# Performance work log

Hardware: AMD Instinct MI355X
Metric: run time of the kernel (lower is better)

## Reference

```python
import jax, jax.numpy as jnp
import numpy as np

B, L, H = 16, 2048, 1024
N = B * L
K_SEL = 8192
LN_EPS = 1e-12
PD_EPS = 1e-6  # torch f.pairwise_distance default eps


def setup_inputs() -> dict:
    key = jax.random.key(0)
    k1, k2, k3, k4 = jax.random.split(key, 4)
    msp = jax.random.normal(k1, (B, L, H), dtype=jnp.float32)
    lab = jax.random.normal(k2, (B, L, H), dtype=jnp.float32)
    # mask with exactly K_SEL true positions (static compaction size)
    perm = jax.random.permutation(k3, N)[:K_SEL]
    mask = jnp.zeros((N,), dtype=bool).at[perm].set(True).reshape(B, L)
    dense_w = jax.random.normal(k4, (H, H), dtype=jnp.float32) / np.sqrt(H)
    return {
        "masked_sentence_prediction": msp,
        "label_embeddings": lab,
        "label_mask": mask,
        "dense_w": dense_w,
        "dense_b": jnp.zeros((H,), dtype=jnp.float32),
        "ln_gamma": jnp.ones((H,), dtype=jnp.float32),
        "ln_beta": jnp.zeros((H,), dtype=jnp.float32),
        "K": K_SEL,
    }


def reference(masked_sentence_prediction, label_embeddings, label_mask,
              dense_w, dense_b, ln_gamma, ln_beta, K):
    Hd = masked_sentence_prediction.shape[-1]
    mask_flat = label_mask.reshape(-1)
    # stream compaction: rows where mask is true (static size K)
    idx = jnp.nonzero(mask_flat, size=K)[0]
    preds = masked_sentence_prediction.reshape(-1, Hd)[idx]      # [K, H]
    labels = label_embeddings.reshape(-1, Hd)[idx]               # [K, H]
    # dense + LayerNorm
    h = preds @ dense_w.T + dense_b
    mu = jnp.mean(h, axis=-1, keepdims=True)
    var = jnp.mean(jnp.square(h - mu), axis=-1, keepdims=True)
    h = (h - mu) * jax.lax.rsqrt(var + LN_EPS) * ln_gamma + ln_beta
    # contrastive logits against dynamic sentence vocabulary
    logits = h @ labels.T                                        # [K, K]
    log_probs = jax.nn.log_softmax(logits, axis=1)
    probs = jnp.exp(log_probs)
    eye = jnp.eye(K, dtype=logits.dtype)
    per_example_loss_distance = jnp.sum(jnp.abs(probs - eye + PD_EPS), axis=1)
    per_example_loss_product = -jnp.diagonal(log_probs)
    denom = K + 1e-5
    loss_distance = jnp.sum(per_example_loss_distance) / denom
    loss_product = jnp.sum(per_example_loss_product) / denom
    loss_variance_distance = jnp.var(per_example_loss_distance, ddof=1)
    loss_variance_product = jnp.var(per_example_loss_product, ddof=1)
    return (logits, per_example_loss_distance, per_example_loss_product,
            loss_distance, loss_product, loss_variance_distance, loss_variance_product)
```

## Files before the change

### kernel.cpp

```cpp
#include <hip/hip_runtime.h>
#include <cstdint>

#define NROWS 32768
#define HD    1024
#define KSEL  8192
#define LN_EPS 1e-12f
#define PD_EPS 1e-6f

typedef unsigned short u16;
typedef __bf16 bf16x8 __attribute__((ext_vector_type(8)));
typedef float  f32x4  __attribute__((ext_vector_type(4)));

__device__ inline u16 f2bf(float f) {
    union { float f; uint32_t u; } x; x.f = f;
    uint32_t r = (x.u + 0x7fffu + ((x.u >> 16) & 1u)) >> 16;
    return (u16)r;
}

__device__ inline uint2 pack4(float a, float b, float c, float d) {
    uint2 r;
    r.x = (uint32_t)f2bf(a) | ((uint32_t)f2bf(b) << 16);
    r.y = (uint32_t)f2bf(c) | ((uint32_t)f2bf(d) << 16);
    return r;
}

__global__ void compact_mask_k(const uint8_t* mb, const int32_t* mi, int* idx) {
    __shared__ int cnt[1024];
    __shared__ int tmp[1024];
    __shared__ int mode_s;
    const int t = threadIdx.x;
    const int per = NROWS / 1024;
    const int base = t * per;
    int c0 = 0;
    for (int i = 0; i < per; ++i) c0 += (mb[base + i] != 0);
    tmp[t] = c0;
    __syncthreads();
    for (int off = 512; off > 0; off >>= 1) {
        if (t < off) tmp[t] += tmp[t + off];
        __syncthreads();
    }
    if (t == 0) mode_s = (tmp[0] == KSEL) ? 0 : 1;
    __syncthreads();
    const int mode = mode_s;
    int c = c0;
    if (mode) { c = 0; for (int i = 0; i < per; ++i) c += (mi[base + i] != 0); }
    cnt[t] = c;
    __syncthreads();
    for (int off = 1; off < 1024; off <<= 1) {
        int add = (t >= off) ? cnt[t - off] : 0;
        __syncthreads();
        cnt[t] += add;
        __syncthreads();
    }
    int pos = cnt[t] - c;
    for (int i = 0; i < per; ++i) {
        bool v = mode ? (mi[base + i] != 0) : (mb[base + i] != 0);
        if (v) idx[pos++] = base + i;
    }
}

__global__ void gather_conv_k(const float* __restrict__ msp, const float* __restrict__ lab,
                              const int* __restrict__ idx, const float* __restrict__ W,
                              u16* __restrict__ predsB, u16* __restrict__ labelsB,
                              u16* __restrict__ Wb) {
    const int b = blockIdx.x;
    const int t = threadIdx.x;
    if (b < KSEL) {
        const int src = idx[b];
        float4 p = *(const float4*)(msp + (size_t)src * HD + t * 4);
        float4 q = *(const float4*)(lab + (size_t)src * HD + t * 4);
        *(uint2*)(predsB  + (size_t)b * HD + t * 4) = pack4(p.x, p.y, p.z, p.w);
        *(uint2*)(labelsB + (size_t)b * HD + t * 4) = pack4(q.x, q.y, q.z, q.w);
    } else {
        const int i = ((b - KSEL) * 256 + t) * 4;
        float4 v = *(const float4*)(W + i);
        *(uint2*)(Wb + i) = pack4(v.x, v.y, v.z, v.w);
    }
}

#define STAGE(XPTR, ROWBASE, KT, I, LBASE) do {                                      \
    const int f_ = (I) * 512 + tid;                                                  \
    const int r_ = f_ >> 3;                                                          \
    const int sp_ = (f_ & 7) ^ (r_ & 7);                                             \
    const u16* g_ = (XPTR) + (size_t)((ROWBASE) + r_) * Kd + koff + (KT) * 64 + sp_ * 8; \
    __builtin_amdgcn_global_load_lds(                                                \
        (const __attribute__((address_space(1))) void*)g_,                           \
        (__attribute__((address_space(3))) void*)(lds + (LBASE) + f_ * 8), 16, 0, 0);\
} while (0)

#define GEMM_PRO_AND_KLOOP(TVAL)                                                      \
    const int nx  = N >> 8;                                                           \
    int wg  = ((nwg & 7) == 0) ? ((bid & 7) * (nwg >> 3) + (bid >> 3)) : bid;         \
    const int bm = wg / nx, bn = wg % nx;                                             \
    const size_t brow = (size_t)bm << 8, bcol = (size_t)bn << 8;                      \
    const int tid = threadIdx.x;                                                      \
    const int l = tid & 63, wid = tid >> 6;                                           \
    const int wm = wid >> 2, wn = wid & 3;                                            \
    const int lr = l & 15, lq = l >> 4;                                               \
    const int sw = lr & 7;                                                            \
    f32x4 acc[8][4] = {};                                                             \
    const int arow = (wm * 128 + lr) * 64;                                            \
    const int brow2 = (wn * 64 + lr) * 64;                                            \
    const int s0 = (lq ^ sw) * 8;                                                     \
    const int s1 = ((4 + lq) ^ sw) * 8;                                               \
    _Pragma("unroll")                                                                 \
    for (int i = 0; i < 4; ++i) STAGE(A,  brow, 0, i, 0);                             \
    _Pragma("unroll")                                                                 \
    for (int i = 0; i < 4; ++i) STAGE(Bt, bcol, 0, i, 49152);                         \
    _Pragma("unroll")                                                                 \
    for (int i = 0; i < 4; ++i) STAGE(A,  brow, 1, i, 16384);                         \
    asm volatile("s_waitcnt vmcnt(4)" ::: "memory");                                  \
    __builtin_amdgcn_s_barrier();                                                     \
    const int T = (TVAL);                                                             \
    int abi = 0;                                                                      \
    _Pragma("unroll 1")                                                               \
    for (int t = 0; t < T; ++t) {                                                     \
        const int aB = abi * 16384;                                                   \
        const int bB = 49152 + (t & 1) * 16384;                                       \
        const int aN = (abi >= 1 ? abi - 1 : 2) * 16384;                              \
        const int bN = 49152 + ((t + 1) & 1) * 16384;                                 \
        bf16x8 a0[8], b0[4], a1[8], b1[4];                                            \
                     \
        _Pragma("unroll")                                                             \
        for (int mi = 0; mi < 8; ++mi)                                                \
            a0[mi] = *(const bf16x8*)(lds + aB + arow + mi * 1024 + s0);              \
        _Pragma("unroll")                                                             \
        for (int ni = 0; ni < 4; ++ni)                                                \
            b0[ni] = *(const bf16x8*)(lds + bB + brow2 + ni * 1024 + s0);             \
        _Pragma("unroll")                                                             \
        for (int mi = 0; mi < 8; ++mi)                                                \
            a1[mi] = *(const bf16x8*)(lds + aB + arow + mi * 1024 + s1);              \
        _Pragma("unroll")                                                             \
        for (int ni = 0; ni < 4; ++ni)                                                \
            b1[ni] = *(const bf16x8*)(lds + bB + brow2 + ni * 1024 + s1);             \
                      \
        if (t + 1 < T) {                                                              \
            STAGE(Bt, bcol, t + 1, 0, bN); STAGE(Bt, bcol, t + 1, 1, bN);             \
            STAGE(Bt, bcol, t + 1, 2, bN); STAGE(Bt, bcol, t + 1, 3, bN);             \
        }                                                                             \
        if (t + 2 < T) {                                                              \
            STAGE(A, brow, t + 2, 0, aN); STAGE(A, brow, t + 2, 1, aN);               \
            STAGE(A, brow, t + 2, 2, aN); STAGE(A, brow, t + 2, 3, aN);               \
        }                                                                             \
                     \
        _Pragma("unroll")                                                             \
        for (int mi = 0; mi < 8; ++mi) {                                              \
            _Pragma("unroll")                                                         \
            for (int ni = 0; ni < 4; ++ni)                                            \
                acc[mi][ni] = __builtin_amdgcn_mfma_f32_16x16x32_bf16(a0[mi], b0[ni], acc[mi][ni], 0, 0, 0); \
        }                                                                             \
        _Pragma("unroll")                                                             \
        for (int mi = 0; mi < 8; ++mi) {                                              \
            _Pragma("unroll")                                                         \
            for (int ni = 0; ni < 4; ++ni)                                            \
                acc[mi][ni] = __builtin_amdgcn_mfma_f32_16x16x32_bf16(a1[mi], b1[ni], acc[mi][ni], 0, 0, 0); \
        }                                                                             \
                      \
        if (t < T - 2) { asm volatile("s_waitcnt vmcnt(4)" ::: "memory"); }           \
        else           { asm volatile("s_waitcnt vmcnt(0)" ::: "memory"); }           \
        __builtin_amdgcn_s_barrier();                                                 \
        abi = (abi == 2) ? 0 : abi + 1;                                               \
    }

__global__ __launch_bounds__(512, 2)
void gemm256a_k(const u16* __restrict__ A, const u16* __restrict__ Bt,
                float* __restrict__ C, int M, int N, int Kd) {
    extern __shared__ u16 lds[];
    const int nwg = (M >> 8) * (N >> 8);
    int bid = blockIdx.x;
    const int half = (bid >= nwg) ? 1 : 0;
    if (half) bid -= nwg;
    const int KdH = Kd >> 1;
    const int koff = half * KdH;
    float* Cp = C + (size_t)half * ((size_t)M * N);
    GEMM_PRO_AND_KLOOP(KdH >> 6);
    #pragma unroll
    for (int m = 0; m < 8; ++m) {
        const size_t rb = brow + wm * 128 + m * 16 + lq * 4;
        #pragma unroll
        for (int n = 0; n < 4; ++n) {
            const size_t cb = bcol + wn * 64 + n * 16 + lr;
            #pragma unroll
            for (int rr = 0; rr < 4; ++rr)
                Cp[(rb + rr) * (size_t)N + cb] = acc[m][n][rr];
        }
    }
}

__global__ __launch_bounds__(512, 2)
void gemm256s_k(const u16* __restrict__ A, const u16* __restrict__ Bt,
                float* __restrict__ C, int M, int N, int Kd,
                float2* __restrict__ pst) {
    extern __shared__ u16 lds[];
    const int nwg = (M >> 8) * (N >> 8);
    int bid = blockIdx.x;
    const int koff = 0;
    GEMM_PRO_AND_KLOOP(Kd >> 6);

    float2* sbuf = (float2*)lds;
    #pragma unroll
    for (int m = 0; m < 8; ++m) {
        #pragma unroll
        for (int rr = 0; rr < 4; ++rr) {
            float v0 = acc[m][0][rr], v1 = acc[m][1][rr];
            float v2 = acc[m][2][rr], v3 = acc[m][3][rr];
            float mx = fmaxf(fmaxf(v0, v1), fmaxf(v2, v3));
            #pragma unroll
            for (int o = 1; o < 16; o <<= 1) mx = fmaxf(mx, __shfl_xor(mx, o));
            float se = __expf(v0 - mx) + __expf(v1 - mx) + __expf(v2 - mx) + __expf(v3 - mx);
            #pragma unroll
            for (int o = 1; o < 16; o <<= 1) se += __shfl_xor(se, o);
            if (lr == 0) {
                const int rl = wm * 128 + m * 16 + lq * 4 + rr;
                sbuf[rl * 5 + wn] = make_float2(mx, se);
            }
        }
        const size_t rb = brow + wm * 128 + m * 16 + lq * 4;
        #pragma unroll
        for (int n = 0; n < 4; ++n) {
            const size_t cb = bcol + wn * 64 + n * 16 + lr;
            #pragma unroll
            for (int rr = 0; rr < 4; ++rr)
                C[(rb + rr) * (size_t)N + cb] = acc[m][n][rr];
        }
    }
    asm volatile("s_waitcnt lgkmcnt(0)" ::: "memory");
    __builtin_amdgcn_s_barrier();
    if (tid < 256) {
        const float2 p0 = sbuf[tid * 5 + 0], p1 = sbuf[tid * 5 + 1];
        const float2 p2 = sbuf[tid * 5 + 2], p3 = sbuf[tid * 5 + 3];
        const float M2 = fmaxf(fmaxf(p0.x, p1.x), fmaxf(p2.x, p3.x));
        const float S2 = p0.y * __expf(p0.x - M2) + p1.y * __expf(p1.x - M2)
                       + p2.y * __expf(p2.x - M2) + p3.y * __expf(p3.x - M2);
        pst[(brow + tid) * (N >> 8) + bn] = make_float2(M2, S2);
    }
}

__global__ __launch_bounds__(256)
void loss_final_k(const float2* __restrict__ pst, const float* __restrict__ logits,
                  float* __restrict__ peld, float* __restrict__ pelp) {
    const int tid = threadIdx.x;
    const int wv = tid >> 6, half = (tid & 63) >> 5, l5 = tid & 31;
    const int row = blockIdx.x * 8 + wv * 2 + half;
    const float2 p = pst[(size_t)row * 32 + l5];
    const float d = logits[(size_t)row * (KSEL + 1)];
    float M = p.x;
    #pragma unroll
    for (int o = 1; o < 32; o <<= 1) M = fmaxf(M, __shfl_xor(M, o));
    float S = p.y * __expf(p.x - M);
    #pragma unroll
    for (int o = 1; o < 32; o <<= 1) S += __shfl_xor(S, o);
    if (l5 == 0) {
        const float pi = __expf(d - M) / S;
        peld[row] = 2.0f - 2.0f * pi + (float)(KSEL - 2) * PD_EPS;
        pelp[row] = M + __logf(S) - d;
    }
}

__device__ inline float blockSum(float v, float* red) {
    #pragma unroll
    for (int o = 32; o > 0; o >>= 1) v += __shfl_down(v, o);
    __syncthreads();
    if ((threadIdx.x & 63) == 0) red[threadIdx.x >> 6] = v;
    __syncthreads();
    return red[0] + red[1] + red[2] + red[3];
}

__global__ void ln_k(const float* __restrict__ Hp0, const float* __restrict__ Hp1,
                     const float* __restrict__ bias,
                     const float* __restrict__ gamma, const float* __restrict__ beta,
                     u16* __restrict__ Hb) {
    __shared__ float red[4];
    const int r = blockIdx.x, t = threadIdx.x;
    float4 x4 = *(const float4*)(Hp0 + (size_t)r * HD + t * 4);
    float4 y4 = *(const float4*)(Hp1 + (size_t)r * HD + t * 4);
    float4 b4 = *(const float4*)(bias + t * 4);
    float x[4] = { x4.x + y4.x + b4.x, x4.y + y4.y + b4.y,
                   x4.z + y4.z + b4.z, x4.w + y4.w + b4.w };
    float s = x[0] + x[1] + x[2] + x[3];
    float mu = blockSum(s, red) * (1.0f / HD);
    float d0 = x[0] - mu, d1 = x[1] - mu, d2 = x[2] - mu, d3 = x[3] - mu;
    float vs = d0 * d0 + d1 * d1 + d2 * d2 + d3 * d3;
    float var = blockSum(vs, red) * (1.0f / HD);
    float rs = rsqrtf(var + LN_EPS);
    float4 g4 = *(const float4*)(gamma + t * 4);
    float4 e4 = *(const float4*)(beta + t * 4);
    float y0 = d0 * rs * g4.x + e4.x;
    float y1 = d1 * rs * g4.y + e4.y;
    float y2 = d2 * rs * g4.z + e4.z;
    float y3 = d3 * rs * g4.w + e4.w;
    *(uint2*)(Hb + (size_t)r * HD + t * 4) = pack4(y0, y1, y2, y3);
}

__global__ __launch_bounds__(1024)
void reduce_k(const float* __restrict__ peld, const float* __restrict__ pelp,
              float* __restrict__ scalars) {
    __shared__ double red[4][16];
    const int t = threadIdx.x;
    double a = 0.0, b = 0.0, c = 0.0, d = 0.0;
    for (int i = t; i < KSEL; i += 1024) {
        const double pd = (double)peld[i];
        const double pp = (double)pelp[i];
        a += pd; b += pd * pd; c += pp; d += pp * pp;
    }
    #pragma unroll
    for (int o = 32; o > 0; o >>= 1) {
        a += __shfl_down(a, o); b += __shfl_down(b, o);
        c += __shfl_down(c, o); d += __shfl_down(d, o);
    }
    const int wv = t >> 6;
    if ((t & 63) == 0) { red[0][wv] = a; red[1][wv] = b; red[2][wv] = c; red[3][wv] = d; }
    __syncthreads();
    if (t == 0) {
        double s1 = 0, s2 = 0, s3 = 0, s4 = 0;
        #pragma unroll
        for (int i = 0; i < 16; ++i) { s1 += red[0][i]; s2 += red[1][i]; s3 += red[2][i]; s4 += red[3][i]; }
        const double Kd = (double)KSEL;
        const double denom = Kd + 1e-5;
        scalars[0] = (float)(s1 / denom);
        scalars[1] = (float)(s3 / denom);
        scalars[2] = (float)((s2 - s1 * s1 / Kd) / (Kd - 1.0));
        scalars[3] = (float)((s4 - s3 * s3 / Kd) / (Kd - 1.0));
    }
}

extern "C" void kernel_launch(void* const* d_in, const int* in_sizes, int n_in,
                              void* d_out, int out_size, void* d_ws, size_t ws_size,
                              hipStream_t stream) {
    const float* msp   = (const float*)d_in[0];
    const float* lab   = (const float*)d_in[1];
    const void*  mask  = d_in[2];
    const float* W     = (const float*)d_in[3];
    const float* bias  = (const float*)d_in[4];
    const float* gamma = (const float*)d_in[5];
    const float* beta  = (const float*)d_in[6];
    float* out = (float*)d_out;
    char*  ws  = (char*)d_ws;

    int*    idx     = (int*)ws;
    float2* pst     = (float2*)(ws + 65536);
    u16*    wBf     = (u16*)(ws + 65536);
    u16*    labelsB = (u16*)(ws + (size_t)(4  << 20));
    u16*    hB      = (u16*)(ws + (size_t)(20 << 20));
    u16*    predsB  = (u16*)d_out;
    float*  hPre    = out + ((size_t)8 << 20);

    float* peld    = out + (size_t)KSEL * KSEL;
    float* pelp    = peld + KSEL;
    float* scalars = pelp + KSEL;

    hipFuncSetAttribute(reinterpret_cast<const void*>(&gemm256a_k),
                        hipFuncAttributeMaxDynamicSharedMemorySize, 163840);
    hipFuncSetAttribute(reinterpret_cast<const void*>(&gemm256s_k),
                        hipFuncAttributeMaxDynamicSharedMemorySize, 163840);

    compact_mask_k<<<1, 1024, 0, stream>>>((const uint8_t*)mask, (const int32_t*)mask, idx);
    gather_conv_k<<<KSEL + 1024, 256, 0, stream>>>(msp, lab, idx, W, predsB, labelsB, wBf);
    gemm256a_k<<<2 * (KSEL / 256) * (HD / 256), 512, 163840, stream>>>(
        predsB, wBf, hPre, KSEL, HD, HD);
    ln_k<<<KSEL, 256, 0, stream>>>(hPre, hPre + (size_t)KSEL * HD, bias, gamma, beta, hB);
    gemm256s_k<<<(KSEL / 256) * (KSEL / 256), 512, 163840, stream>>>(
        hB, labelsB, out, KSEL, KSEL, HD, pst);
    loss_final_k<<<KSEL / 8, 256, 0, stream>>>(pst, out, peld, pelp);
    reduce_k<<<1, 1024, 0, stream>>>(peld, pelp, scalars);
}
```

Before: 266.7 us.

## Run logits GEMM in FP8 e4m3 instead of bf16

Normalized hidden states and label embeddings are now packed to FP8 e4m3 rather than bf16, and the KxK logits GEMM uses fp8 MFMA with K-tiles of 128 bytes per row. The shared GEMM macro is inlined into the dense GEMM and a separate FP8 staging and loop path is written for the logits GEMM. The aim is to halve the bytes moved and raise MFMA throughput for the dominant GEMM. In exchange, logits precision drops sharply, which risks the accuracy of the outputs and the softmax-derived losses.

```diff
diff --git a/kernel.cpp b/kernel.cpp
--- a/kernel.cpp
+++ b/kernel.cpp
@@ -22,6 +22,34 @@
     r.x = (uint32_t)f2bf(a) | ((uint32_t)f2bf(b) << 16);
     r.y = (uint32_t)f2bf(c) | ((uint32_t)f2bf(d) << 16);
     return r;
+}
+
+__device__ inline uint32_t enc_e4m3(float f) {
+    union { float f; uint32_t u; } x; x.f = f;
+    uint32_t s = (x.u >> 31) << 7;
+    float a = fabsf(f);
+    if (a >= 448.f) return s | 0x7e;
+    if (a < 0.001953125f) {
+        int q = (int)(a * 512.f + 0.5f);
+        return s | (uint32_t)q;
+    }
+    int e; float m = frexpf(a, &e);
+    int E = e - 1 + 7;
+    int q = (int)((m * 2.f - 1.f) * 8.f + 0.5f);
+    if (q == 8) { q = 0; E += 1; }
+    if (E >= 16) return s | 0x7e;
+    if (E <= 0) { int qq = (int)(a * 512.f + 0.5f); return s | (uint32_t)qq; }
+    return s | (uint32_t)(E << 3) | (uint32_t)q;
+}
+
+__device__ inline uint32_t pack4_f8(float a, float b, float c, float d) {
+#if defined(__has_builtin) && __has_builtin(__builtin_amdgcn_cvt_pk_fp8_f32)
+    int v = __builtin_amdgcn_cvt_pk_fp8_f32(a, b, 0, false);
+    v = __builtin_amdgcn_cvt_pk_fp8_f32(c, d, v, true);
+    return (uint32_t)v;
+#else
+    return enc_e4m3(a) | (enc_e4m3(b) << 8) | (enc_e4m3(c) << 16) | (enc_e4m3(d) << 24);
+#endif
 }
 
 __global__ void compact_mask_k(const uint8_t* mb, const int32_t* mi, int* idx) {
@@ -61,7 +89,7 @@
 
 __global__ void gather_conv_k(const float* __restrict__ msp, const float* __restrict__ lab,
                               const int* __restrict__ idx, const float* __restrict__ W,
-                              u16* __restrict__ predsB, u16* __restrict__ labelsB,
+                              u16* __restrict__ predsB, uint8_t* __restrict__ labelsB8,
                               u16* __restrict__ Wb) {
     const int b = blockIdx.x;
     const int t = threadIdx.x;
@@ -69,8 +97,8 @@
         const int src = idx[b];
         float4 p = *(const float4*)(msp + (size_t)src * HD + t * 4);
         float4 q = *(const float4*)(lab + (size_t)src * HD + t * 4);
-        *(uint2*)(predsB  + (size_t)b * HD + t * 4) = pack4(p.x, p.y, p.z, p.w);
-        *(uint2*)(labelsB + (size_t)b * HD + t * 4) = pack4(q.x, q.y, q.z, q.w);
+        *(uint2*)(predsB + (size_t)b * HD + t * 4) = pack4(p.x, p.y, p.z, p.w);
+        *(uint32_t*)(labelsB8 + (size_t)b * HD + t * 4) = pack4_f8(q.x, q.y, q.z, q.w);
     } else {
         const int i = ((b - KSEL) * 256 + t) * 4;
         float4 v = *(const float4*)(W + i);
@@ -87,80 +115,6 @@
         (const __attribute__((address_space(1))) void*)g_,                           \
         (__attribute__((address_space(3))) void*)(lds + (LBASE) + f_ * 8), 16, 0, 0);\
 } while (0)
-
-#define GEMM_PRO_AND_KLOOP(TVAL)                                                      \
-    const int nx  = N >> 8;                                                           \
-    int wg  = ((nwg & 7) == 0) ? ((bid & 7) * (nwg >> 3) + (bid >> 3)) : bid;         \
-    const int bm = wg / nx, bn = wg % nx;                                             \
-    const size_t brow = (size_t)bm << 8, bcol = (size_t)bn << 8;                      \
-    const int tid = threadIdx.x;                                                      \
-    const int l = tid & 63, wid = tid >> 6;                                           \
-    const int wm = wid >> 2, wn = wid & 3;                                            \
-    const int lr = l & 15, lq = l >> 4;                                               \
-    const int sw = lr & 7;                                                            \
-    f32x4 acc[8][4] = {};                                                             \
-    const int arow = (wm * 128 + lr) * 64;                                            \
-    const int brow2 = (wn * 64 + lr) * 64;                                            \
-    const int s0 = (lq ^ sw) * 8;                                                     \
-    const int s1 = ((4 + lq) ^ sw) * 8;                                               \
-    _Pragma("unroll")                                                                 \
-    for (int i = 0; i < 4; ++i) STAGE(A,  brow, 0, i, 0);                             \
-    _Pragma("unroll")                                                                 \
-    for (int i = 0; i < 4; ++i) STAGE(Bt, bcol, 0, i, 49152);                         \
-    _Pragma("unroll")                                                                 \
-    for (int i = 0; i < 4; ++i) STAGE(A,  brow, 1, i, 16384);                         \
-    asm volatile("s_waitcnt vmcnt(4)" ::: "memory");                                  \
-    __builtin_amdgcn_s_barrier();                                                     \
-    const int T = (TVAL);                                                             \
-    int abi = 0;                                                                      \
-    _Pragma("unroll 1")                                                               \
-    for (int t = 0; t < T; ++t) {                                                     \
-        const int aB = abi * 16384;                                                   \
-        const int bB = 49152 + (t & 1) * 16384;                                       \
-        const int aN = (abi >= 1 ? abi - 1 : 2) * 16384;                              \
-        const int bN = 49152 + ((t + 1) & 1) * 16384;                                 \
-        bf16x8 a0[8], b0[4], a1[8], b1[4];                                            \
-                     \
-        _Pragma("unroll")                                                             \
-        for (int mi = 0; mi < 8; ++mi)                                                \
-            a0[mi] = *(const bf16x8*)(lds + aB + arow + mi * 1024 + s0);              \
-        _Pragma("unroll")                                                             \
-        for (int ni = 0; ni < 4; ++ni)                                                \
-            b0[ni] = *(const bf16x8*)(lds + bB + brow2 + ni * 1024 + s0);             \
-        _Pragma("unroll")                                                             \
-        for (int mi = 0; mi < 8; ++mi)                                                \
-            a1[mi] = *(const bf16x8*)(lds + aB + arow + mi * 1024 + s1);              \
-        _Pragma("unroll")                                                             \
-        for (int ni = 0; ni < 4; ++ni)                                                \
-            b1[ni] = *(const bf16x8*)(lds + bB + brow2 + ni * 1024 + s1);             \
-                      \
-        if (t + 1 < T) {                                                              \
-            STAGE(Bt, bcol, t + 1, 0, bN); STAGE(Bt, bcol, t + 1, 1, bN);             \
-            STAGE(Bt, bcol, t + 1, 2, bN); STAGE(Bt, bcol, t + 1, 3, bN);             \
-        }                                                                             \
-        if (t + 2 < T) {                                                              \
-            STAGE(A, brow, t + 2, 0, aN); STAGE(A, brow, t + 2, 1, aN);               \
-            STAGE(A, brow, t + 2, 2, aN); STAGE(A, brow, t + 2, 3, aN);               \
-        }                                                                             \
-                     \
-        _Pragma("unroll")                                                             \
-        for (int mi = 0; mi < 8; ++mi) {                                              \
-            _Pragma("unroll")                                                         \
-            for (int ni = 0; ni < 4; ++ni)                                            \
-                acc[mi][ni] = __builtin_amdgcn_mfma_f32_16x16x32_bf16(a0[mi], b0[ni], acc[mi][ni], 0, 0, 0); \
-        }                                                                             \
-        _Pragma("unroll")                                                             \
-        for (int mi = 0; mi < 8; ++mi) {                                              \
-            _Pragma("unroll")                                                         \
-            for (int ni = 0; ni < 4; ++ni)                                            \
-                acc[mi][ni] = __builtin_amdgcn_mfma_f32_16x16x32_bf16(a1[mi], b1[ni], acc[mi][ni], 0, 0, 0); \
-        }                                                                             \
-                      \
-        if (t < T - 2) { asm volatile("s_waitcnt vmcnt(4)" ::: "memory"); }           \
-        else           { asm volatile("s_waitcnt vmcnt(0)" ::: "memory"); }           \
-        __builtin_amdgcn_s_barrier();                                                 \
-        abi = (abi == 2) ? 0 : abi + 1;                                               \
-    }
 
 __global__ __launch_bounds__(512, 2)
 void gemm256a_k(const u16* __restrict__ A, const u16* __restrict__ Bt,
@@ -173,7 +127,75 @@
     const int KdH = Kd >> 1;
     const int koff = half * KdH;
     float* Cp = C + (size_t)half * ((size_t)M * N);
-    GEMM_PRO_AND_KLOOP(KdH >> 6);
+
+    const int nx  = N >> 8;
+    int wg  = ((nwg & 7) == 0) ? ((bid & 7) * (nwg >> 3) + (bid >> 3)) : bid;
+    const int bm = wg / nx, bn = wg % nx;
+    const size_t brow = (size_t)bm << 8, bcol = (size_t)bn << 8;
+    const int tid = threadIdx.x;
+    const int l = tid & 63, wid = tid >> 6;
+    const int wm = wid >> 2, wn = wid & 3;
+    const int lr = l & 15, lq = l >> 4;
+    const int sw = lr & 7;
+    f32x4 acc[8][4] = {};
+    const int arow = (wm * 128 + lr) * 64;
+    const int brow2 = (wn * 64 + lr) * 64;
+    const int s0 = (lq ^ sw) * 8;
+    const int s1 = ((4 + lq) ^ sw) * 8;
+    #pragma unroll
+    for (int i = 0; i < 4; ++i) STAGE(A,  brow, 0, i, 0);
+    #pragma unroll
+    for (int i = 0; i < 4; ++i) STAGE(Bt, bcol, 0, i, 49152);
+    #pragma unroll
+    for (int i = 0; i < 4; ++i) STAGE(A,  brow, 1, i, 16384);
+    asm volatile("s_waitcnt vmcnt(4)" ::: "memory");
+    __builtin_amdgcn_s_barrier();
+    const int T = KdH >> 6;
+    int abi = 0;
+    #pragma unroll 1
+    for (int t = 0; t < T; ++t) {
+        const int aB = abi * 16384;
+        const int bB = 49152 + (t & 1) * 16384;
+        const int aN = (abi >= 1 ? abi - 1 : 2) * 16384;
+        const int bN = 49152 + ((t + 1) & 1) * 16384;
+        bf16x8 a0[8], b0[4], a1[8], b1[4];
+        #pragma unroll
+        for (int mi = 0; mi < 8; ++mi)
+            a0[mi] = *(const bf16x8*)(lds + aB + arow + mi * 1024 + s0);
+        #pragma unroll
+        for (int ni = 0; ni < 4; ++ni)
+            b0[ni] = *(const bf16x8*)(lds + bB + brow2 + ni * 1024 + s0);
+        #pragma unroll
+        for (int mi = 0; mi < 8; ++mi)
+            a1[mi] = *(const bf16x8*)(lds + aB + arow + mi * 1024 + s1);
+        #pragma unroll
+        for (int ni = 0; ni < 4; ++ni)
+            b1[ni] = *(const bf16x8*)(lds + bB + brow2 + ni * 1024 + s1);
+        if (t + 1 < T) {
+            STAGE(Bt, bcol, t + 1, 0, bN); STAGE(Bt, bcol, t + 1, 1, bN);
+            STAGE(Bt, bcol, t + 1, 2, bN); STAGE(Bt, bcol, t + 1, 3, bN);
+        }
+        if (t + 2 < T) {
+            STAGE(A, brow, t + 2, 0, aN); STAGE(A, brow, t + 2, 1, aN);
+            STAGE(A, brow, t + 2, 2, aN); STAGE(A, brow, t + 2, 3, aN);
+        }
+        #pragma unroll
+        for (int mi = 0; mi < 8; ++mi) {
+            #pragma unroll
+            for (int ni = 0; ni < 4; ++ni)
+                acc[mi][ni] = __builtin_amdgcn_mfma_f32_16x16x32_bf16(a0[mi], b0[ni], acc[mi][ni], 0, 0, 0);
+        }
+        #pragma unroll
+        for (int mi = 0; mi < 8; ++mi) {
+            #pragma unroll
+            for (int ni = 0; ni < 4; ++ni)
+                acc[mi][ni] = __builtin_amdgcn_mfma_f32_16x16x32_bf16(a1[mi], b1[ni], acc[mi][ni], 0, 0, 0);
+        }
+        if (t < T - 2) { asm volatile("s_waitcnt vmcnt(4)" ::: "memory"); }
+        else           { asm volatile("s_waitcnt vmcnt(0)" ::: "memory"); }
+        __builtin_amdgcn_s_barrier();
+        abi = (abi == 2) ? 0 : abi + 1;
+    }
     #pragma unroll
     for (int m = 0; m < 8; ++m) {
         const size_t rb = brow + wm * 128 + m * 16 + lq * 4;
@@ -187,17 +209,90 @@
     }
 }
 
+#define STAGE8(XPTR, ROWBASE, KT, I, LBASE) do {                                     \
+    const int f_ = (I) * 512 + tid;                                                  \
+    const int r_ = f_ >> 3;                                                          \
+    const int sp_ = (f_ & 7) ^ (r_ & 7);                                             \
+    const uint8_t* g_ = (XPTR) + (size_t)((ROWBASE) + r_) * Kd + (KT) * 128 + sp_ * 16; \
+    __builtin_amdgcn_global_load_lds(                                                \
+        (const __attribute__((address_space(1))) void*)g_,                           \
+        (__attribute__((address_space(3))) void*)(lds8 + (LBASE) + f_ * 16), 16, 0, 0);\
+} while (0)
+
 __global__ __launch_bounds__(512, 2)
-void gemm256s_k(const u16* __restrict__ A, const u16* __restrict__ Bt,
+void gemm256s_k(const uint8_t* __restrict__ A, const uint8_t* __restrict__ Bt,
                 float* __restrict__ C, int M, int N, int Kd,
                 float2* __restrict__ pst) {
     extern __shared__ u16 lds[];
-    const int nwg = (M >> 8) * (N >> 8);
+    uint8_t* lds8 = (uint8_t*)lds;
+    const int nx  = N >> 8;
+    const int nwg = (M >> 8) * nx;
     int bid = blockIdx.x;
-    const int koff = 0;
-    GEMM_PRO_AND_KLOOP(Kd >> 6);
-
-    float2* sbuf = (float2*)lds;
+    int wg  = ((nwg & 7) == 0) ? ((bid & 7) * (nwg >> 3) + (bid >> 3)) : bid;
+    const int bm = wg / nx, bn = wg % nx;
+    const size_t brow = (size_t)bm << 8, bcol = (size_t)bn << 8;
+    const int tid = threadIdx.x;
+    const int l = tid & 63, wid = tid >> 6;
+    const int wm = wid >> 2, wn = wid & 3;
+    const int lr = l & 15, lq = l >> 4;
+    const int sw = lr & 7;
+    f32x4 acc[8][4] = {};
+    const int arow = (wm * 128 + lr) * 128;
+    const int brow2 = (wn * 64 + lr) * 128;
+    int fo[4];
+    #pragma unroll
+    for (int kk = 0; kk < 4; ++kk)
+        fo[kk] = (((kk * 2 + (lq >> 1)) ^ sw) * 16) + (lq & 1) * 8;
+
+    #pragma unroll
+    for (int i = 0; i < 4; ++i) STAGE8(A,  brow, 0, i, 0);
+    #pragma unroll
+    for (int i = 0; i < 4; ++i) STAGE8(Bt, bcol, 0, i, 98304);
+    #pragma unroll
+    for (int i = 0; i < 4; ++i) STAGE8(A,  brow, 1, i, 32768);
+    asm volatile("s_waitcnt vmcnt(4)" ::: "memory");
+    __builtin_amdgcn_s_barrier();
+
+    const int T = Kd >> 7;
+    int abi = 0;
+    #pragma unroll 1
+    for (int t = 0; t < T; ++t) {
+        const int aB = abi * 32768;
+        const int bB = 98304 + (t & 1) * 32768;
+        const int aN = (abi >= 1 ? abi - 1 : 2) * 32768;
+        const int bN = 98304 + ((t + 1) & 1) * 32768;
+        if (t + 1 < T) {
+            STAGE8(Bt, bcol, t + 1, 0, bN); STAGE8(Bt, bcol, t + 1, 1, bN);
+            STAGE8(Bt, bcol, t + 1, 2, bN); STAGE8(Bt, bcol, t + 1, 3, bN);
+        }
+        if (t + 2 < T) {
+            STAGE8(A, brow, t + 2, 0, aN); STAGE8(A, brow, t + 2, 1, aN);
+            STAGE8(A, brow, t + 2, 2, aN); STAGE8(A, brow, t + 2, 3, aN);
+        }
+        #pragma unroll
+        for (int kk = 0; kk < 4; ++kk) {
+            long a[8], b[4];
+            #pragma unroll
+            for (int mi = 0; mi < 8; ++mi)
+                a[mi] = *(const long*)(lds8 + aB + arow + mi * 2048 + fo[kk]);
+            #pragma unroll
+            for (int ni = 0; ni < 4; ++ni)
+                b[ni] = *(const long*)(lds8 + bB + brow2 + ni * 2048 + fo[kk]);
+            #pragma unroll
+            for (int mi = 0; mi < 8; ++mi) {
+                #pragma unroll
+                for (int ni = 0; ni < 4; ++ni)
+                    acc[mi][ni] = __builtin_amdgcn_mfma_f32_16x16x32_fp8_fp8(
+                        a[mi], b[ni], acc[mi][ni], 0, 0, 0);
+            }
+        }
+        if (t < T - 2) { asm volatile("s_waitcnt vmcnt(4)" ::: "memory"); }
+        else           { asm volatile("s_waitcnt vmcnt(0)" ::: "memory"); }
+        __builtin_amdgcn_s_barrier();
+        abi = (abi == 2) ? 0 : abi + 1;
+    }
+
+    float2* sbuf = (float2*)lds8;
     #pragma unroll
     for (int m = 0; m < 8; ++m) {
         #pragma unroll
@@ -269,7 +364,7 @@
 __global__ void ln_k(const float* __restrict__ Hp0, const float* __restrict__ Hp1,
                      const float* __restrict__ bias,
                      const float* __restrict__ gamma, const float* __restrict__ beta,
-                     u16* __restrict__ Hb) {
+                     uint8_t* __restrict__ Hb8) {
     __shared__ float red[4];
     const int r = blockIdx.x, t = threadIdx.x;
     float4 x4 = *(const float4*)(Hp0 + (size_t)r * HD + t * 4);
@@ -289,7 +384,7 @@
     float y1 = d1 * rs * g4.y + e4.y;
     float y2 = d2 * rs * g4.z + e4.z;
     float y3 = d3 * rs * g4.w + e4.w;
-    *(uint2*)(Hb + (size_t)r * HD + t * 4) = pack4(y0, y1, y2, y3);
+    *(uint32_t*)(Hb8 + (size_t)r * HD + t * 4) = pack4_f8(y0, y1, y2, y3);
 }
 
 __global__ __launch_bounds__(1024)
@@ -337,13 +432,13 @@
     float* out = (float*)d_out;
     char*  ws  = (char*)d_ws;
 
-    int*    idx     = (int*)ws;
-    float2* pst     = (float2*)(ws + 65536);
-    u16*    wBf     = (u16*)(ws + 65536);
-    u16*    labelsB = (u16*)(ws + (size_t)(4  << 20));
-    u16*    hB      = (u16*)(ws + (size_t)(20 << 20));
-    u16*    predsB  = (u16*)d_out;
-    float*  hPre    = out + ((size_t)8 << 20);
+    int*     idx      = (int*)ws;
+    float2*  pst      = (float2*)(ws + 65536);
+    u16*     wBf      = (u16*)(ws + 65536);
+    uint8_t* labelsB8 = (uint8_t*)(ws + (size_t)(4  << 20));
+    uint8_t* hB8      = (uint8_t*)(ws + (size_t)(20 << 20));
+    u16*     predsB   = (u16*)d_out;
+    float*   hPre     = out + ((size_t)8 << 20);
 
     float* peld    = out + (size_t)KSEL * KSEL;
     float* pelp    = peld + KSEL;
@@ -355,12 +450,12 @@
                         hipFuncAttributeMaxDynamicSharedMemorySize, 163840);
 
     compact_mask_k<<<1, 1024, 0, stream>>>((const uint8_t*)mask, (const int32_t*)mask, idx);
-    gather_conv_k<<<KSEL + 1024, 256, 0, stream>>>(msp, lab, idx, W, predsB, labelsB, wBf);
+    gather_conv_k<<<KSEL + 1024, 256, 0, stream>>>(msp, lab, idx, W, predsB, labelsB8, wBf);
     gemm256a_k<<<2 * (KSEL / 256) * (HD / 256), 512, 163840, stream>>>(
         predsB, wBf, hPre, KSEL, HD, HD);
-    ln_k<<<KSEL, 256, 0, stream>>>(hPre, hPre + (size_t)KSEL * HD, bias, gamma, beta, hB);
+    ln_k<<<KSEL, 256, 0, stream>>>(hPre, hPre + (size_t)KSEL * HD, bias, gamma, beta, hB8);
     gemm256s_k<<<(KSEL / 256) * (KSEL / 256), 512, 163840, stream>>>(
-        hB, labelsB, out, KSEL, KSEL, HD, pst);
+        hB8, labelsB8, out, KSEL, KSEL, HD, pst);
     loss_final_k<<<KSEL / 8, 256, 0, stream>>>(pst, out, peld, pelp);
     reduce_k<<<1, 1024, 0, stream>>>(peld, pelp, scalars);
 }
```

After: 255.5 us. -4.2%, faster.

## Switch both GEMMs from bf16 to fp8 e4m3 scaled MFMA

Applied to the files above, without the earlier changes.

Converts gathered preds, labels, weights and LayerNorm output to fp8 e4m3 instead of bf16, and runs both GEMMs with the 16x16x128 f8f6f4 scaled MFMA using unit scales. LDS staging is reworked for 128-byte K tiles, so each tile covers twice the K depth and the K-loop runs half as many iterations. This halves operand bandwidth and doubles MFMA throughput per instruction. The cost is much lower precision: fp8 with 3 mantissa bits may push the logits and softmax-derived losses outside tolerance.

```diff
diff --git a/kernel.cpp b/kernel.cpp
--- a/kernel.cpp
+++ b/kernel.cpp
@@ -8,20 +8,36 @@
 #define PD_EPS 1e-6f
 
 typedef unsigned short u16;
-typedef __bf16 bf16x8 __attribute__((ext_vector_type(8)));
 typedef float  f32x4  __attribute__((ext_vector_type(4)));
-
-__device__ inline u16 f2bf(float f) {
+typedef int    v8i    __attribute__((ext_vector_type(8)));
+typedef int    v4i    __attribute__((ext_vector_type(4)));
+
+__device__ inline uint32_t enc_e4m3(float f) {
     union { float f; uint32_t u; } x; x.f = f;
-    uint32_t r = (x.u + 0x7fffu + ((x.u >> 16) & 1u)) >> 16;
-    return (u16)r;
-}
-
-__device__ inline uint2 pack4(float a, float b, float c, float d) {
-    uint2 r;
-    r.x = (uint32_t)f2bf(a) | ((uint32_t)f2bf(b) << 16);
-    r.y = (uint32_t)f2bf(c) | ((uint32_t)f2bf(d) << 16);
-    return r;
+    uint32_t s = (x.u >> 31) << 7;
+    float a = fabsf(f);
+    if (a >= 448.f) return s | 0x7e;
+    if (a < 0.001953125f) {
+        int q = (int)(a * 512.f + 0.5f);
+        return s | (uint32_t)q;
+    }
+    int e; float m = frexpf(a, &e);
+    int E = e - 1 + 7;
+    int q = (int)((m * 2.f - 1.f) * 8.f + 0.5f);
+    if (q == 8) { q = 0; E += 1; }
+    if (E >= 16) return s | 0x7e;
+    if (E <= 0) { int qq = (int)(a * 512.f + 0.5f); return s | (uint32_t)qq; }
+    return s | (uint32_t)(E << 3) | (uint32_t)q;
+}
+
+__device__ inline uint32_t pack4_f8(float a, float b, float c, float d) {
+#if defined(__has_builtin) && __has_builtin(__builtin_amdgcn_cvt_pk_fp8_f32)
+    int v = __builtin_amdgcn_cvt_pk_fp8_f32(a, b, 0, false);
+    v = __builtin_amdgcn_cvt_pk_fp8_f32(c, d, v, true);
+    return (uint32_t)v;
+#else
+    return enc_e4m3(a) | (enc_e4m3(b) << 8) | (enc_e4m3(c) << 16) | (enc_e4m3(d) << 24);
+#endif
 }
 
 __global__ void compact_mask_k(const uint8_t* mb, const int32_t* mi, int* idx) {
@@ -61,34 +77,43 @@
 
 __global__ void gather_conv_k(const float* __restrict__ msp, const float* __restrict__ lab,
                               const int* __restrict__ idx, const float* __restrict__ W,
-                              u16* __restrict__ predsB, u16* __restrict__ labelsB,
-                              u16* __restrict__ Wb) {
+                              uint8_t* __restrict__ predsB8, uint8_t* __restrict__ labelsB8,
+                              uint8_t* __restrict__ Wb8) {
     const int b = blockIdx.x;
     const int t = threadIdx.x;
     if (b < KSEL) {
         const int src = idx[b];
         float4 p = *(const float4*)(msp + (size_t)src * HD + t * 4);
         float4 q = *(const float4*)(lab + (size_t)src * HD + t * 4);
-        *(uint2*)(predsB  + (size_t)b * HD + t * 4) = pack4(p.x, p.y, p.z, p.w);
-        *(uint2*)(labelsB + (size_t)b * HD + t * 4) = pack4(q.x, q.y, q.z, q.w);
+        *(uint32_t*)(predsB8  + (size_t)b * HD + t * 4) = pack4_f8(p.x, p.y, p.z, p.w);
+        *(uint32_t*)(labelsB8 + (size_t)b * HD + t * 4) = pack4_f8(q.x, q.y, q.z, q.w);
     } else {
         const int i = ((b - KSEL) * 256 + t) * 4;
         float4 v = *(const float4*)(W + i);
-        *(uint2*)(Wb + i) = pack4(v.x, v.y, v.z, v.w);
-    }
-}
-
-#define STAGE(XPTR, ROWBASE, KT, I, LBASE) do {                                      \
+        *(uint32_t*)(Wb8 + i) = pack4_f8(v.x, v.y, v.z, v.w);
+    }
+}
+
+#define STAGE8(XPTR, ROWBASE, KT, I, LBASE) do {                                     \
     const int f_ = (I) * 512 + tid;                                                  \
     const int r_ = f_ >> 3;                                                          \
     const int sp_ = (f_ & 7) ^ (r_ & 7);                                             \
-    const u16* g_ = (XPTR) + (size_t)((ROWBASE) + r_) * Kd + koff + (KT) * 64 + sp_ * 8; \
+    const uint8_t* g_ = (XPTR) + (size_t)((ROWBASE) + r_) * Kd + koff + (KT) * 128 + sp_ * 16; \
     __builtin_amdgcn_global_load_lds(                                                \
         (const __attribute__((address_space(1))) void*)g_,                           \
-        (__attribute__((address_space(3))) void*)(lds + (LBASE) + f_ * 8), 16, 0, 0);\
+        (__attribute__((address_space(3))) void*)(lds8 + (LBASE) + f_ * 16), 16, 0, 0);\
 } while (0)
 
-#define GEMM_PRO_AND_KLOOP(TVAL)                                                      \
+__device__ inline v8i ld_frag32(const uint8_t* p0, const uint8_t* p1) {
+    v4i lo = *(const v4i*)p0;
+    v4i hi = *(const v4i*)p1;
+    v8i r;
+    r[0] = lo[0]; r[1] = lo[1]; r[2] = lo[2]; r[3] = lo[3];
+    r[4] = hi[0]; r[5] = hi[1]; r[6] = hi[2]; r[7] = hi[3];
+    return r;
+}
+
+#define FP8_GEMM_BODY(TVAL)                                                           \
     const int nx  = N >> 8;                                                           \
     int wg  = ((nwg & 7) == 0) ? ((bid & 7) * (nwg >> 3) + (bid >> 3)) : bid;         \
     const int bm = wg / nx, bn = wg % nx;                                             \
@@ -99,63 +124,51 @@
     const int lr = l & 15, lq = l >> 4;                                               \
     const int sw = lr & 7;                                                            \
     f32x4 acc[8][4] = {};                                                             \
-    const int arow = (wm * 128 + lr) * 64;                                            \
-    const int brow2 = (wn * 64 + lr) * 64;                                            \
-    const int s0 = (lq ^ sw) * 8;                                                     \
-    const int s1 = ((4 + lq) ^ sw) * 8;                                               \
+    const int arow = (wm * 128 + lr) * 128;                                           \
+    const int brow2 = (wn * 64 + lr) * 128;                                           \
+    const int f0 = ((lq * 2 + 0) ^ sw) * 16;                                          \
+    const int f1 = ((lq * 2 + 1) ^ sw) * 16;                                          \
     _Pragma("unroll")                                                                 \
-    for (int i = 0; i < 4; ++i) STAGE(A,  brow, 0, i, 0);                             \
+    for (int i = 0; i < 4; ++i) STAGE8(A,  brow, 0, i, 0);                            \
     _Pragma("unroll")                                                                 \
-    for (int i = 0; i < 4; ++i) STAGE(Bt, bcol, 0, i, 49152);                         \
+    for (int i = 0; i < 4; ++i) STAGE8(Bt, bcol, 0, i, 98304);                        \
     _Pragma("unroll")                                                                 \
-    for (int i = 0; i < 4; ++i) STAGE(A,  brow, 1, i, 16384);                         \
+    for (int i = 0; i < 4; ++i) STAGE8(A,  brow, 1, i, 32768);                        \
     asm volatile("s_waitcnt vmcnt(4)" ::: "memory");                                  \
     __builtin_amdgcn_s_barrier();                                                     \
     const int T = (TVAL);                                                             \
     int abi = 0;                                                                      \
     _Pragma("unroll 1")                                                               \
     for (int t = 0; t < T; ++t) {                                                     \
-        const int aB = abi * 16384;                                                   \
-        const int bB = 49152 + (t & 1) * 16384;                                       \
-        const int aN = (abi >= 1 ? abi - 1 : 2) * 16384;                              \
-        const int bN = 49152 + ((t + 1) & 1) * 16384;                                 \
-        bf16x8 a0[8], b0[4], a1[8], b1[4];                                            \
-                     \
+        const int aB = abi * 32768;                                                   \
+        const int bB = 98304 + (t & 1) * 32768;                                       \
+        const int aN = (abi >= 1 ? abi - 1 : 2) * 32768;                              \
+        const int bN = 98304 + ((t + 1) & 1) * 32768;                                 \
+        v8i a8[8], b8[4];                                                             \
         _Pragma("unroll")                                                             \
         for (int mi = 0; mi < 8; ++mi)                                                \
-            a0[mi] = *(const bf16x8*)(lds + aB + arow + mi * 1024 + s0);              \
+            a8[mi] = ld_frag32(lds8 + aB + arow + mi * 2048 + f0,                     \
+                               lds8 + aB + arow + mi * 2048 + f1);                    \
         _Pragma("unroll")                                                             \
         for (int ni = 0; ni < 4; ++ni)                                                \
-            b0[ni] = *(const bf16x8*)(lds + bB + brow2 + ni * 1024 + s0);             \
-        _Pragma("unroll")                                                             \
-        for (int mi = 0; mi < 8; ++mi)                                                \
-            a1[mi] = *(const bf16x8*)(lds + aB + arow + mi * 1024 + s1);              \
-        _Pragma("unroll")                                                             \
-        for (int ni = 0; ni < 4; ++ni)                                                \
-            b1[ni] = *(const bf16x8*)(lds + bB + brow2 + ni * 1024 + s1);             \
-                      \
+            b8[ni] = ld_frag32(lds8 + bB + brow2 + ni * 2048 + f0,                    \
+                               lds8 + bB + brow2 + ni * 2048 + f1);                   \
         if (t + 1 < T) {                                                              \
-            STAGE(Bt, bcol, t + 1, 0, bN); STAGE(Bt, bcol, t + 1, 1, bN);             \
-            STAGE(Bt, bcol, t + 1, 2, bN); STAGE(Bt, bcol, t + 1, 3, bN);             \
+            STAGE8(Bt, bcol, t + 1, 0, bN); STAGE8(Bt, bcol, t + 1, 1, bN);           \
+            STAGE8(Bt, bcol, t + 1, 2, bN); STAGE8(Bt, bcol, t + 1, 3, bN);           \
         }                                                                             \
         if (t + 2 < T) {                                                              \
-            STAGE(A, brow, t + 2, 0, aN); STAGE(A, brow, t + 2, 1, aN);               \
-            STAGE(A, brow, t + 2, 2, aN); STAGE(A, brow, t + 2, 3, aN);               \
-        }                                                                             \
-                     \
-        _Pragma("unroll")                                                             \
-        for (int mi = 0; mi < 8; ++mi) {                                              \
-            _Pragma("unroll")                                                         \
-            for (int ni = 0; ni < 4; ++ni)                                            \
-                acc[mi][ni] = __builtin_amdgcn_mfma_f32_16x16x32_bf16(a0[mi], b0[ni], acc[mi][ni], 0, 0, 0); \
+            STAGE8(A, brow, t + 2, 0, aN); STAGE8(A, brow, t + 2, 1, aN);             \
+            STAGE8(A, brow, t + 2, 2, aN); STAGE8(A, brow, t + 2, 3, aN);             \
         }                                                                             \
         _Pragma("unroll")                                                             \
         for (int mi = 0; mi < 8; ++mi) {                                              \
             _Pragma("unroll")                                                         \
             for (int ni = 0; ni < 4; ++ni)                                            \
-                acc[mi][ni] = __builtin_amdgcn_mfma_f32_16x16x32_bf16(a1[mi], b1[ni], acc[mi][ni], 0, 0, 0); \
+                acc[mi][ni] = __builtin_amdgcn_mfma_scale_f32_16x16x128_f8f6f4(       \
+                    a8[mi], b8[ni], acc[mi][ni],                                      \
+                    0, 0, 0, 0x7f7f7f7f, 0, 0x7f7f7f7f);                              \
         }                                                                             \
-                      \
         if (t < T - 2) { asm volatile("s_waitcnt vmcnt(4)" ::: "memory"); }           \
         else           { asm volatile("s_waitcnt vmcnt(0)" ::: "memory"); }           \
         __builtin_amdgcn_s_barrier();                                                 \
@@ -163,9 +176,10 @@
     }
 
 __global__ __launch_bounds__(512, 2)
-void gemm256a_k(const u16* __restrict__ A, const u16* __restrict__ Bt,
+void gemm256a_k(const uint8_t* __restrict__ A, const uint8_t* __restrict__ Bt,
                 float* __restrict__ C, int M, int N, int Kd) {
     extern __shared__ u16 lds[];
+    uint8_t* lds8 = (uint8_t*)lds;
     const int nwg = (M >> 8) * (N >> 8);
     int bid = blockIdx.x;
     const int half = (bid >= nwg) ? 1 : 0;
@@ -173,7 +187,7 @@
     const int KdH = Kd >> 1;
     const int koff = half * KdH;
     float* Cp = C + (size_t)half * ((size_t)M * N);
-    GEMM_PRO_AND_KLOOP(KdH >> 6);
+    FP8_GEMM_BODY(KdH >> 7);
     #pragma unroll
     for (int m = 0; m < 8; ++m) {
         const size_t rb = brow + wm * 128 + m * 16 + lq * 4;
@@ -188,16 +202,17 @@
 }
 
 __global__ __launch_bounds__(512, 2)
-void gemm256s_k(const u16* __restrict__ A, const u16* __restrict__ Bt,
+void gemm256s_k(const uint8_t* __restrict__ A, const uint8_t* __restrict__ Bt,
                 float* __restrict__ C, int M, int N, int Kd,
                 float2* __restrict__ pst) {
     extern __shared__ u16 lds[];
+    uint8_t* lds8 = (uint8_t*)lds;
     const int nwg = (M >> 8) * (N >> 8);
     int bid = blockIdx.x;
     const int koff = 0;
-    GEMM_PRO_AND_KLOOP(Kd >> 6);
-
-    float2* sbuf = (float2*)lds;
+    FP8_GEMM_BODY(Kd >> 7);
+
+    float2* sbuf = (float2*)lds8;
     #pragma unroll
     for (int m = 0; m < 8; ++m) {
         #pragma unroll
@@ -269,7 +284,7 @@
 __global__ void ln_k(const float* __restrict__ Hp0, const float* __restrict__ Hp1,
                      const float* __restrict__ bias,
                      const float* __restrict__ gamma, const float* __restrict__ beta,
-                     u16* __restrict__ Hb) {
+                     uint8_t* __restrict__ Hb8) {
     __shared__ float red[4];
     const int r = blockIdx.x, t = threadIdx.x;
     float4 x4 = *(const float4*)(Hp0 + (size_t)r * HD + t * 4);
@@ -289,7 +304,7 @@
     float y1 = d1 * rs * g4.y + e4.y;
     float y2 = d2 * rs * g4.z + e4.z;
     float y3 = d3 * rs * g4.w + e4.w;
-    *(uint2*)(Hb + (size_t)r * HD + t * 4) = pack4(y0, y1, y2, y3);
+    *(uint32_t*)(Hb8 + (size_t)r * HD + t * 4) = pack4_f8(y0, y1, y2, y3);
 }
 
 __global__ __launch_bounds__(1024)
@@ -337,13 +352,13 @@
     float* out = (float*)d_out;
     char*  ws  = (char*)d_ws;
 
-    int*    idx     = (int*)ws;
-    float2* pst     = (float2*)(ws + 65536);
-    u16*    wBf     = (u16*)(ws + 65536);
-    u16*    labelsB = (u16*)(ws + (size_t)(4  << 20));
-    u16*    hB      = (u16*)(ws + (size_t)(20 << 20));
-    u16*    predsB  = (u16*)d_out;
-    float*  hPre    = out + ((size_t)8 << 20);
+    int*     idx      = (int*)ws;
+    uint8_t* wB8      = (uint8_t*)(ws + 65536);
+    float2*  pst      = (float2*)(ws + 65536);
+    uint8_t* labelsB8 = (uint8_t*)(ws + (size_t)(4  << 20));
+    uint8_t* hB8      = (uint8_t*)(ws + (size_t)(20 << 20));
+    uint8_t* predsB8  = (uint8_t*)d_out;
+    float*   hPre     = out + ((size_t)8 << 20);
 
     float* peld    = out + (size_t)KSEL * KSEL;
     float* pelp    = peld + KSEL;
@@ -355,12 +370,12 @@
                         hipFuncAttributeMaxDynamicSharedMemorySize, 163840);
 
     compact_mask_k<<<1, 1024, 0, stream>>>((const uint8_t*)mask, (const int32_t*)mask, idx);
-    gather_conv_k<<<KSEL + 1024, 256, 0, stream>>>(msp, lab, idx, W, predsB, labelsB, wBf);
+    gather_conv_k<<<KSEL + 1024, 256, 0, stream>>>(msp, lab, idx, W, predsB8, labelsB8, wB8);
     gemm256a_k<<<2 * (KSEL / 256) * (HD / 256), 512, 163840, stream>>>(
-        predsB, wBf, hPre, KSEL, HD, HD);
-    ln_k<<<KSEL, 256, 0, stream>>>(hPre, hPre + (size_t)KSEL * HD, bias, gamma, beta, hB);
+        predsB8, wB8, hPre, KSEL, HD, HD);
+    ln_k<<<KSEL, 256, 0, stream>>>(hPre, hPre + (size_t)KSEL * HD, bias, gamma, beta, hB8);
     gemm256s_k<<<(KSEL / 256) * (KSEL / 256), 512, 163840, stream>>>(
-        hB, labelsB, out, KSEL, KSEL, HD, pst);
+        hB8, labelsB8, out, KSEL, KSEL, HD, pst);
     loss_final_k<<<KSEL / 8, 256, 0, stream>>>(pst, out, peld, pelp);
     reduce_k<<<1, 1024, 0, stream>>>(peld, pelp, scalars);
 }
```

Result: faster. 224.9 us (-15.7%).
